# Optimization experiments

Hardware: AMD Instinct MI355X
Metric: run time of the kernel (lower is better)

Reference implementation:

```python
import jax, jax.numpy as jnp
import numpy as np

S, B, H = 2048, 2, 2048
NP = 16            # num attention heads
HN = H // NP       # head dim = 128


def setup_inputs() -> dict:
    key = jax.random.key(0)
    k0, k1, k2 = jax.random.split(key, 3)
    hidden_states = jax.random.normal(k0, (S, B, H), dtype=jnp.float32) * 0.02
    w_qkv = jax.random.normal(k1, (3 * H, H), dtype=jnp.float32) * 0.02
    b_qkv = jnp.zeros((3 * H,), dtype=jnp.float32)
    w_dense = jax.random.normal(k2, (H, H), dtype=jnp.float32) * 0.02
    b_dense = jnp.zeros((H,), dtype=jnp.float32)
    # causal mask: True means "mask out" (strictly upper triangular)
    attention_mask = jnp.triu(jnp.ones((S, S), dtype=bool), k=1)[None, None]  # [1,1,S,S]
    return {
        "hidden_states": hidden_states,
        "attention_mask": attention_mask,
        "w_qkv": w_qkv,
        "b_qkv": b_qkv,
        "w_dense": w_dense,
        "b_dense": b_dense,
    }


def reference(hidden_states, attention_mask, w_qkv, b_qkv, w_dense, b_dense):
    s, b, h = hidden_states.shape
    # fused QKV projection (ColumnParallelLinear: y = x @ W^T + b)
    mixed = hidden_states @ w_qkv.T + b_qkv                 # [s,b,3h]
    mixed = mixed.reshape(s, b, NP, 3 * HN)
    q, k, v = jnp.split(mixed, 3, axis=-1)                  # each [s,b,np,hn]
    norm = 1.0 / jnp.sqrt(jnp.asarray(HN, hidden_states.dtype))
    # scaled QK^T -> [b,np,sq,sk]
    scores = jnp.einsum("sbnh,tbnh->bnst", q, k) * norm
    # attention_mask_func: masked_fill(mask, -10000.0)
    scores = jnp.where(attention_mask, jnp.asarray(-10000.0, scores.dtype), scores)
    # softmax in fp32 (softmax_in_fp32)
    probs = jax.nn.softmax(scores.astype(jnp.float32), axis=-1).astype(scores.dtype)
    # AV matmul -> [s,b,np,hn] -> [s,b,h]
    context = jnp.einsum("bnst,tbnh->sbnh", probs, v).reshape(s, b, h)
    # output projection (RowParallelLinear)
    out = context @ w_dense.T + b_dense
    return out
```

## Files before the change

### kernel.cpp

```cpp
#include <hip/hip_runtime.h>
#include <hip/hip_bf16.h>
#include <cstdint>
#include <cstddef>

#define SS   2048
#define BB   2
#define HH   2048
#define NHEAD 16
#define HDIM 128
#define H3   6144
#define MROWS 4096

typedef __attribute__((ext_vector_type(4))) float f32x4;
typedef __attribute__((ext_vector_type(8))) __bf16 bf16x8;
typedef __attribute__((ext_vector_type(8))) unsigned short us8;
typedef __attribute__((ext_vector_type(4))) unsigned short us4;

__device__ __forceinline__ unsigned short f2b(float f) {
    union { float f; unsigned u; } v; v.f = f;
    unsigned r = v.u + 0x7fffu + ((v.u >> 16) & 1u);
    return (unsigned short)(r >> 16);
}

__device__ __forceinline__ bf16x8 ld_b16x8(const unsigned short* p) {
    us8 u = *(const us8*)p;
    return __builtin_bit_cast(bf16x8, u);
}

__device__ __forceinline__ bf16x8 ld8_off(const unsigned short* base, int byteoff) {
    return __builtin_bit_cast(bf16x8, *(const us8*)((const char*)base + byteoff));
}

__device__ __forceinline__ int sw256(int b) { return b ^ (((b >> 8) & 7) << 4); }
__device__ __forceinline__ int sw128(int b) { return b ^ (((b >> 7) & 7) << 4); }

__device__ __forceinline__ void gload_lds16(const unsigned short* g, unsigned short* l) {
    __builtin_amdgcn_global_load_lds(
        (const __attribute__((address_space(1))) unsigned int*)g,
        (__attribute__((address_space(3))) unsigned int*)l, 16, 0, 0);
}

__global__ __launch_bounds__(256) void cvt_f32_bf16(
    const float* __restrict__ in, unsigned short* __restrict__ out, int n4)
{
    const int stride = gridDim.x * blockDim.x;
    for (int i = blockIdx.x * blockDim.x + threadIdx.x; i < n4; i += stride) {
        const float4 v = ((const float4*)in)[i];
        us4 o = { f2b(v.x), f2b(v.y), f2b(v.z), f2b(v.w) };
        ((us4*)out)[i] = o;
    }
}

__global__ __launch_bounds__(256) void transpose_v(
    const unsigned short* __restrict__ mixed,
    unsigned short* __restrict__ vt)
{
    const int st = blockIdx.x;
    const int nh = blockIdx.y;
    const int bb = blockIdx.z;
    const int tid = threadIdx.x;
    __shared__ unsigned short T[64][136];
#pragma unroll
    for (int i = 0; i < 4; ++i) {
        const int c = i * 256 + tid;
        const int sl = c >> 4, d0 = (c & 15) << 3;
        const us8 v = *(const us8*)(mixed +
            ((size_t)(st * 64 + sl) * BB + bb) * H3 + nh * 384 + 256 + d0);
        *(us8*)(&T[sl][d0]) = v;
    }
    __syncthreads();
#pragma unroll
    for (int i = 0; i < 4; ++i) {
        const int c = i * 256 + tid;
        const int d = c >> 3, sl0 = (c & 7) << 3;
        us8 o;
#pragma unroll
        for (int j = 0; j < 8; ++j) o[j] = T[sl0 + j][d];
        *(us8*)(vt + ((size_t)(bb * NHEAD + nh) * HDIM + d) * SS + st * 64 + sl0) = o;
    }
}

#define STAGE_UNIT(gp, lo)                                        \
    gload_lds16((gp) + soff[0], smem + (lo) + tid * 8);           \
    gload_lds16((gp) + soff[1], smem + (lo) + 4096 + tid * 8);

template <int BN, bool F32OUT>
__global__ __launch_bounds__(512, 2) void gemm_8ph(
    const unsigned short* __restrict__ A,
    const unsigned short* __restrict__ Bw,
    const float* __restrict__ bias,
    void* __restrict__ Cout,
    int Nv, int Kv)
{
    extern __shared__ unsigned short smem[];
    constexpr int NF     = BN / 64;
    constexpr int BUNITS = BN / 128;
    constexpr int BELEMS = BN * 64;

    const int tid  = threadIdx.x;
    const int lane = tid & 63;
    const int wave = tid >> 6;
    const int wm = wave >> 2, wn = wave & 3;
    const int bm = blockIdx.y, bn = blockIdx.x;

    const unsigned short* Ab = A  + (size_t)bm * 128 * Kv;
    const unsigned short* Bb = Bw + (size_t)bn * BN * Kv;

    int soff[2];
#pragma unroll
    for (int i = 0; i < 2; ++i) {
        const int p = (i * 512 + tid) * 16;
        const int l = p ^ (((p >> 7) & 7) << 4);
        soff[i] = (l >> 7) * Kv + ((l & 127) >> 1);
    }

    f32x4 acc[4][NF];
#pragma unroll
    for (int m = 0; m < 4; ++m)
#pragma unroll
        for (int n = 0; n < NF; ++n) acc[m][n] = (f32x4){0.f, 0.f, 0.f, 0.f};

    const int frow = lane & 15;
    const int g16  = (lane >> 4) << 4;
    const int swx  = (frow & 7) << 4;
    const int kx0  = g16 ^ swx;
    const int kx1  = (64 + g16) ^ swx;
    const int aRow = (wm * 64 + frow) * 128;
    const int bRow = 32768 + (wn * (BN / 4) + frow) * 128;

    const int NT = Kv >> 6;

    STAGE_UNIT(Ab, 0);
    STAGE_UNIT(Bb, 16384);
    STAGE_UNIT(Bb + 128 * Kv, 16384 + 8192);
    if constexpr (BUNITS == 3) { STAGE_UNIT(Bb + 256 * Kv, 16384 + 16384); }
    STAGE_UNIT(Bb + 64, 16384 + BELEMS);
    STAGE_UNIT(Bb + 128 * Kv + 64, 16384 + BELEMS + 8192);
    if constexpr (BUNITS == 3) { STAGE_UNIT(Bb + 256 * Kv + 64, 16384 + BELEMS + 16384); }
    if constexpr (BUNITS == 3) { asm volatile("s_waitcnt vmcnt(6)" ::: "memory"); }
    else                       { asm volatile("s_waitcnt vmcnt(4)" ::: "memory"); }
    __builtin_amdgcn_s_barrier();

    for (int t = 0; t < NT; ++t) {
        const int j  = t & 1;
        const int jn = j ^ 1;
        const int aj = j * 16384;
        const int bj = j * (BN * 128);
        const int cA = ((t + 1 < NT) ? (t + 1) : (NT - 1)) * 64;
        const int cB = ((t + 2 < NT) ? (t + 2) : (NT - 1)) * 64;

        bf16x8 bbf[NF][2];

        {
            bf16x8 a0 = ld8_off(smem, aj + aRow + 0 * 2048 + kx0);
            bf16x8 a1 = ld8_off(smem, aj + aRow + 0 * 2048 + kx1);
#pragma unroll
            for (int n = 0; n < NF; ++n) {
                bbf[n][0] = ld8_off(smem, bj + bRow + n * 2048 + kx0);
                bbf[n][1] = ld8_off(smem, bj + bRow + n * 2048 + kx1);
            }
            STAGE_UNIT(Ab + cA, jn * 8192);
            __builtin_amdgcn_s_barrier();
            asm volatile("s_waitcnt lgkmcnt(0)" ::: "memory");
            __builtin_amdgcn_sched_barrier(0);
            __builtin_amdgcn_s_setprio(1);
#pragma unroll
            for (int n = 0; n < NF; ++n) {
                acc[0][n] = __builtin_amdgcn_mfma_f32_16x16x32_bf16(a0, bbf[n][0], acc[0][n], 0, 0, 0);
                acc[0][n] = __builtin_amdgcn_mfma_f32_16x16x32_bf16(a1, bbf[n][1], acc[0][n], 0, 0, 0);
            }
            __builtin_amdgcn_s_setprio(0);
        }
        {
            bf16x8 a0 = ld8_off(smem, aj + aRow + 1 * 2048 + kx0);
            bf16x8 a1 = ld8_off(smem, aj + aRow + 1 * 2048 + kx1);
            STAGE_UNIT(Bb + cB, 16384 + j * BELEMS);
            __builtin_amdgcn_s_barrier();
            asm volatile("s_waitcnt lgkmcnt(0)" ::: "memory");
            __builtin_amdgcn_sched_barrier(0);
            __builtin_amdgcn_s_setprio(1);
#pragma unroll
            for (int n = 0; n < NF; ++n) {
                acc[1][n] = __builtin_amdgcn_mfma_f32_16x16x32_bf16(a0, bbf[n][0], acc[1][n], 0, 0, 0);
                acc[1][n] = __builtin_amdgcn_mfma_f32_16x16x32_bf16(a1, bbf[n][1], acc[1][n], 0, 0, 0);
            }
            __builtin_amdgcn_s_setprio(0);
        }
        {
            bf16x8 a0 = ld8_off(smem, aj + aRow + 2 * 2048 + kx0);
            bf16x8 a1 = ld8_off(smem, aj + aRow + 2 * 2048 + kx1);
            STAGE_UNIT(Bb + 128 * Kv + cB, 16384 + j * BELEMS + 8192);
            __builtin_amdgcn_s_barrier();
            asm volatile("s_waitcnt lgkmcnt(0)" ::: "memory");
            __builtin_amdgcn_sched_barrier(0);
            __builtin_amdgcn_s_setprio(1);
#pragma unroll
            for (int n = 0; n < NF; ++n) {
                acc[2][n] = __builtin_amdgcn_mfma_f32_16x16x32_bf16(a0, bbf[n][0], acc[2][n], 0, 0, 0);
                acc[2][n] = __builtin_amdgcn_mfma_f32_16x16x32_bf16(a1, bbf[n][1], acc[2][n], 0, 0, 0);
            }
            __builtin_amdgcn_s_setprio(0);
        }
        {
            bf16x8 a0 = ld8_off(smem, aj + aRow + 3 * 2048 + kx0);
            bf16x8 a1 = ld8_off(smem, aj + aRow + 3 * 2048 + kx1);
            if constexpr (BUNITS == 3) {
                STAGE_UNIT(Bb + 256 * Kv + cB, 16384 + j * BELEMS + 16384);
            }
            __builtin_amdgcn_s_barrier();
            asm volatile("s_waitcnt lgkmcnt(0)" ::: "memory");
            __builtin_amdgcn_sched_barrier(0);
            __builtin_amdgcn_s_setprio(1);
#pragma unroll
            for (int n = 0; n < NF; ++n) {
                acc[3][n] = __builtin_amdgcn_mfma_f32_16x16x32_bf16(a0, bbf[n][0], acc[3][n], 0, 0, 0);
                acc[3][n] = __builtin_amdgcn_mfma_f32_16x16x32_bf16(a1, bbf[n][1], acc[3][n], 0, 0, 0);
            }
            __builtin_amdgcn_s_setprio(0);
            if constexpr (BUNITS == 3) { asm volatile("s_waitcnt vmcnt(6)" ::: "memory"); }
            else                       { asm volatile("s_waitcnt vmcnt(4)" ::: "memory"); }
        }
    }

    const int r0 = (lane >> 4) << 2;
#pragma unroll
    for (int m = 0; m < 4; ++m) {
        const int row = bm * 128 + wm * 64 + m * 16 + r0;
#pragma unroll
        for (int n = 0; n < NF; ++n) {
            const int col = bn * BN + wn * (BN / 4) + n * 16 + frow;
            const float bv = bias[col];
            float scale = 1.0f;
            if constexpr (!F32OUT) {
                if ((col % 384) < 128) scale = 0.088388347648318447f;
            }
#pragma unroll
            for (int r = 0; r < 4; ++r) {
                const float o = (acc[m][n][r] + bv) * scale;
                if (F32OUT) ((float*)Cout)[(size_t)(row + r) * Nv + col] = o;
                else        ((unsigned short*)Cout)[(size_t)(row + r) * Nv + col] = f2b(o);
            }
        }
    }
}

__global__ __launch_bounds__(256) void attn_kernel(
    const unsigned short* __restrict__ mixed,
    const unsigned short* __restrict__ vt,
    unsigned short* __restrict__ context)
{
    const int pair = blockIdx.x;
    const int nh   = blockIdx.y;
    const int bb   = blockIdx.z;
    const int tid  = threadIdx.x;
    const int lane = tid & 63;
    const int wave = tid >> 6;

    __shared__ __align__(1024) unsigned short smem[16384 + 16384 + 4096];

    const int frow = lane & 15;
    const int g16  = (lane >> 4) << 4;
    const int r0   = (lane >> 4) << 2;

    int koff[4], voff[4];
#pragma unroll
    for (int i = 0; i < 4; ++i) {
        const int p0 = (i * 256 + tid) * 16;
        const int lK = p0 ^ (((p0 >> 8) & 7) << 4);
        koff[i] = (lK >> 8) * (BB * H3) + ((lK & 255) >> 1);
        const int lV = p0 ^ (((p0 >> 7) & 7) << 4);
        voff[i] = (lV >> 7) * SS + ((lV & 127) >> 1);
    }

    const unsigned short* kg = mixed + (size_t)bb * H3 + nh * 384 + 128;
    const unsigned short* vg = vt + (size_t)(bb * NHEAD + nh) * HDIM * SS;

    char* Pb = (char*)(smem + 32768) + wave * 2048;

    for (int half = 0; half < 2; ++half) {
        const int qt = half ? (31 - pair) : pair;
        const int q0 = qt * 64 + wave * 16;

        bf16x8 qf[4];
        {
            const unsigned short* qptr =
                mixed + ((size_t)(q0 + frow) * BB + bb) * H3 + nh * 384;
#pragma unroll
            for (int kk = 0; kk < 4; ++kk)
                qf[kk] = ld_b16x8(qptr + kk * 32 + ((lane >> 4) << 3));
        }

        f32x4 Oacc[8];
#pragma unroll
        for (int ct = 0; ct < 8; ++ct) Oacc[ct] = (f32x4){0.f, 0.f, 0.f, 0.f};
        float m_r[4] = {-1e30f, -1e30f, -1e30f, -1e30f};
        float l_r[4] = {0.f, 0.f, 0.f, 0.f};

        {
            unsigned short* Kd = smem + wave * 512;
            unsigned short* Vd = smem + 16384 + wave * 512;
#pragma unroll
            for (int i = 0; i < 4; ++i) {
                gload_lds16(kg + koff[i], Kd + i * 2048);
                gload_lds16(vg + voff[i], Vd + i * 2048);
            }
        }
        __syncthreads();

        int cur = 0;
        for (int kt = 0; kt <= qt; ++kt) {
            if (kt < qt) {
                const unsigned short* kt_g = kg + (size_t)(kt + 1) * 64 * (BB * H3);
                const unsigned short* vt_g = vg + (kt + 1) * 64;
                unsigned short* Kd = smem + (cur ^ 1) * 8192 + wave * 512;
                unsigned short* Vd = smem + 16384 + (cur ^ 1) * 8192 + wave * 512;
#pragma unroll
                for (int i = 0; i < 4; ++i) {
                    gload_lds16(kt_g + koff[i], Kd + i * 2048);
                    gload_lds16(vt_g + voff[i], Vd + i * 2048);
                }
            }

            const unsigned short* Ks = smem + cur * 8192;
            const unsigned short* Vs = smem + 16384 + cur * 8192;

            f32x4 sc4[4];
#pragma unroll
            for (int t = 0; t < 4; ++t) {
                f32x4 s = (f32x4){0.f, 0.f, 0.f, 0.f};
#pragma unroll
                for (int kk = 0; kk < 4; ++kk) {
                    bf16x8 kf = ld8_off(Ks, sw256((t * 16 + frow) * 256 + kk * 64 + g16));
                    s = __builtin_amdgcn_mfma_f32_16x16x32_bf16(qf[kk], kf, s, 0, 0, 0);
                }
                sc4[t] = s;
            }

            if (kt == qt) {
#pragma unroll
                for (int t = 0; t < 4; ++t) {
                    const int kcol = qt * 64 + t * 16 + frow;
#pragma unroll
                    for (int r = 0; r < 4; ++r)
                        if (kcol > q0 + r0 + r) sc4[t][r] = -1e30f;
                }
            }

            float tmax[4];
#pragma unroll
            for (int r = 0; r < 4; ++r)
                tmax[r] = fmaxf(fmaxf(sc4[0][r], sc4[1][r]), fmaxf(sc4[2][r], sc4[3][r]));
#pragma unroll
            for (int r = 0; r < 4; ++r) {
                tmax[r] = fmaxf(tmax[r], __shfl_xor(tmax[r], 1, 64));
                tmax[r] = fmaxf(tmax[r], __shfl_xor(tmax[r], 2, 64));
                tmax[r] = fmaxf(tmax[r], __shfl_xor(tmax[r], 4, 64));
                tmax[r] = fmaxf(tmax[r], __shfl_xor(tmax[r], 8, 64));
            }

            bool need = false;
#pragma unroll
            for (int r = 0; r < 4; ++r) need = need || (tmax[r] > m_r[r] + 8.0f);
            if (__any(need)) {
                float a_r[4];
#pragma unroll
                for (int r = 0; r < 4; ++r) {
                    const float mnew = fmaxf(m_r[r], tmax[r]);
                    a_r[r] = __expf(m_r[r] - mnew);
                    m_r[r] = mnew;
                    l_r[r] *= a_r[r];
                }
#pragma unroll
                for (int ct = 0; ct < 8; ++ct)
#pragma unroll
                    for (int r = 0; r < 4; ++r) Oacc[ct][r] *= a_r[r];
            }

            float rsum[4] = {0.f, 0.f, 0.f, 0.f};
#pragma unroll
            for (int t = 0; t < 4; ++t)
#pragma unroll
                for (int r = 0; r < 4; ++r) {
                    const float p = __expf(sc4[t][r] - m_r[r]);
                    sc4[t][r] = p;
                    rsum[r] += p;
                }
#pragma unroll
            for (int r = 0; r < 4; ++r) {
                rsum[r] += __shfl_xor(rsum[r], 1, 64);
                rsum[r] += __shfl_xor(rsum[r], 2, 64);
                rsum[r] += __shfl_xor(rsum[r], 4, 64);
                rsum[r] += __shfl_xor(rsum[r], 8, 64);
                l_r[r] += rsum[r];
            }

#pragma unroll
            for (int t = 0; t < 4; ++t)
#pragma unroll
                for (int r = 0; r < 4; ++r)
                    *(unsigned short*)(Pb + sw128((r0 + r) * 128 + (t * 16 + frow) * 2)) =
                        f2b(sc4[t][r]);

#pragma unroll
            for (int ks = 0; ks < 2; ++ks) {
                bf16x8 pf = ld8_off((const unsigned short*)Pb, sw128(frow * 128 + ks * 64 + g16));
#pragma unroll
                for (int ct = 0; ct < 8; ++ct) {
                    bf16x8 vf = ld8_off(Vs, sw128((ct * 16 + frow) * 128 + ks * 64 + g16));
                    Oacc[ct] = __builtin_amdgcn_mfma_f32_16x16x32_bf16(pf, vf, Oacc[ct], 0, 0, 0);
                }
            }

            __syncthreads();
            cur ^= 1;
        }

#pragma unroll
        for (int ct = 0; ct < 8; ++ct) {
            const int d = ct * 16 + frow;
#pragma unroll
            for (int r = 0; r < 4; ++r) {
                const float o = Oacc[ct][r] / l_r[r];
                const size_t row = (size_t)(q0 + r0 + r) * BB + bb;
                context[row * HH + nh * 128 + d] = f2b(o);
            }
        }
    }
}

extern "C" void kernel_launch(void* const* d_in, const int* in_sizes, int n_in,
                              void* d_out, int out_size, void* d_ws, size_t ws_size,
                              hipStream_t stream) {
    const float* hidden  = (const float*)d_in[0];
    const float* w_qkv   = (const float*)d_in[2];
    const float* b_qkv   = (const float*)d_in[3];
    const float* w_dense = (const float*)d_in[4];
    const float* b_dense = (const float*)d_in[5];
    float* out = (float*)d_out;

    unsigned short* mixed = (unsigned short*)d_ws;
    unsigned short* hb    = mixed + (size_t)MROWS * H3;
    unsigned short* wq    = hb + (size_t)MROWS * HH;
    unsigned short* wd    = wq + (size_t)H3 * HH;
    unsigned short* context = hb;
    unsigned short* vtg     = wq;

    dim3 blk(256);
    cvt_f32_bf16<<<2048, blk, 0, stream>>>(hidden, hb, (MROWS * HH) / 4);
    cvt_f32_bf16<<<2048, blk, 0, stream>>>(w_qkv, wq, (H3 * HH) / 4);
    cvt_f32_bf16<<<1024, blk, 0, stream>>>(w_dense, wd, (HH * HH) / 4);

    hipFuncSetAttribute(reinterpret_cast<const void*>(gemm_8ph<384, false>),
                        hipFuncAttributeMaxDynamicSharedMemorySize, 131072);
    gemm_8ph<384, false><<<dim3(H3 / 384, MROWS / 128), dim3(512), 131072, stream>>>(
        hb, wq, b_qkv, mixed, H3, HH);
    transpose_v<<<dim3(32, NHEAD, BB), blk, 0, stream>>>(mixed, vtg);
    attn_kernel<<<dim3(16, NHEAD, BB), blk, 0, stream>>>(mixed, vtg, context);
    hipFuncSetAttribute(reinterpret_cast<const void*>(gemm_8ph<256, true>),
                        hipFuncAttributeMaxDynamicSharedMemorySize, 98304);
    gemm_8ph<256, true><<<dim3(HH / 256, MROWS / 128), dim3(512), 98304, stream>>>(
        context, wd, b_dense, out, HH, HH);
}
```

Measured before the change: 266.2 us.

## Use exp2 with folded log2e scale, lazy rescale reductions, hw bf16 cast, remapped grid

The log2(e) factor is folded into the Q scaling in the QKV GEMM epilogue, so the attention softmax can call raw v_exp_f32 (exp2) instead of __expf. The cross-lane max reduction now runs only when some lane's partial max passes the threshold, and that threshold is raised to 11.5 in log2 units. Software bf16 rounding is replaced with the hardware conversion. The attention grid is flattened to 1D and remapped so that neighbouring blocks land on different head/batch pairs, which is meant to spread work across XCDs. The looser rescale threshold allows larger unnormalised exponentials, which carries some precision risk.

```diff
diff --git a/kernel.cpp b/kernel.cpp
--- a/kernel.cpp
+++ b/kernel.cpp
@@ -20,6 +20,16 @@
     union { float f; unsigned u; } v; v.f = f;
     unsigned r = v.u + 0x7fffu + ((v.u >> 16) & 1u);
     return (unsigned short)(r >> 16);
+}
+
+__device__ __forceinline__ unsigned short f2b_hw(float f) {
+    return __builtin_bit_cast(unsigned short, (__bf16)f);
+}
+
+__device__ __forceinline__ float exp2_fast(float x) {
+    float r;
+    asm("v_exp_f32 %0, %1" : "=v"(r) : "v"(x));
+    return r;
 }
 
 __device__ __forceinline__ bf16x8 ld_b16x8(const unsigned short* p) {
@@ -232,7 +242,8 @@
             const float bv = bias[col];
             float scale = 1.0f;
             if constexpr (!F32OUT) {
-                if ((col % 384) < 128) scale = 0.088388347648318447f;
+                if ((col % 384) < 128)
+                    scale = (float)(0.08838834764831843 * 1.4426950408889634);
             }
 #pragma unroll
             for (int r = 0; r < 4; ++r) {
@@ -249,9 +260,14 @@
     const unsigned short* __restrict__ vt,
     unsigned short* __restrict__ context)
 {
-    const int pair = blockIdx.x;
-    const int nh   = blockIdx.y;
-    const int bb   = blockIdx.z;
+    const int id   = blockIdx.x;
+    const int c    = id & 7;
+    const int k    = id >> 3;
+    const int pair = k & 15;
+    const int nhbb = c + 8 * (k >> 4);
+    const int nh   = nhbb >> 1;
+    const int bb   = nhbb & 1;
+
     const int tid  = threadIdx.x;
     const int lane = tid & 63;
     const int wave = tid >> 6;
@@ -346,27 +362,28 @@
                 }
             }
 
-            float tmax[4];
+            float pmax[4];
 #pragma unroll
             for (int r = 0; r < 4; ++r)
-                tmax[r] = fmaxf(fmaxf(sc4[0][r], sc4[1][r]), fmaxf(sc4[2][r], sc4[3][r]));
-#pragma unroll
-            for (int r = 0; r < 4; ++r) {
-                tmax[r] = fmaxf(tmax[r], __shfl_xor(tmax[r], 1, 64));
-                tmax[r] = fmaxf(tmax[r], __shfl_xor(tmax[r], 2, 64));
-                tmax[r] = fmaxf(tmax[r], __shfl_xor(tmax[r], 4, 64));
-                tmax[r] = fmaxf(tmax[r], __shfl_xor(tmax[r], 8, 64));
-            }
-
+                pmax[r] = fmaxf(fmaxf(sc4[0][r], sc4[1][r]), fmaxf(sc4[2][r], sc4[3][r]));
             bool need = false;
 #pragma unroll
-            for (int r = 0; r < 4; ++r) need = need || (tmax[r] > m_r[r] + 8.0f);
+            for (int r = 0; r < 4; ++r) need = need || (pmax[r] > m_r[r] + 11.5f);
             if (__any(need)) {
+                float tmax[4];
+#pragma unroll
+                for (int r = 0; r < 4; ++r) {
+                    tmax[r] = pmax[r];
+                    tmax[r] = fmaxf(tmax[r], __shfl_xor(tmax[r], 1, 64));
+                    tmax[r] = fmaxf(tmax[r], __shfl_xor(tmax[r], 2, 64));
+                    tmax[r] = fmaxf(tmax[r], __shfl_xor(tmax[r], 4, 64));
+                    tmax[r] = fmaxf(tmax[r], __shfl_xor(tmax[r], 8, 64));
+                }
                 float a_r[4];
 #pragma unroll
                 for (int r = 0; r < 4; ++r) {
                     const float mnew = fmaxf(m_r[r], tmax[r]);
-                    a_r[r] = __expf(m_r[r] - mnew);
+                    a_r[r] = exp2_fast(m_r[r] - mnew);
                     m_r[r] = mnew;
                     l_r[r] *= a_r[r];
                 }
@@ -381,7 +398,7 @@
             for (int t = 0; t < 4; ++t)
 #pragma unroll
                 for (int r = 0; r < 4; ++r) {
-                    const float p = __expf(sc4[t][r] - m_r[r]);
+                    const float p = exp2_fast(sc4[t][r] - m_r[r]);
                     sc4[t][r] = p;
                     rsum[r] += p;
                 }
@@ -399,7 +416,7 @@
 #pragma unroll
                 for (int r = 0; r < 4; ++r)
                     *(unsigned short*)(Pb + sw128((r0 + r) * 128 + (t * 16 + frow) * 2)) =
-                        f2b(sc4[t][r]);
+                        f2b_hw(sc4[t][r]);
 
 #pragma unroll
             for (int ks = 0; ks < 2; ++ks) {
@@ -422,7 +439,7 @@
             for (int r = 0; r < 4; ++r) {
                 const float o = Oacc[ct][r] / l_r[r];
                 const size_t row = (size_t)(q0 + r0 + r) * BB + bb;
-                context[row * HH + nh * 128 + d] = f2b(o);
+                context[row * HH + nh * 128 + d] = f2b_hw(o);
             }
         }
     }
@@ -455,7 +472,7 @@
     gemm_8ph<384, false><<<dim3(H3 / 384, MROWS / 128), dim3(512), 131072, stream>>>(
         hb, wq, b_qkv, mixed, H3, HH);
     transpose_v<<<dim3(32, NHEAD, BB), blk, 0, stream>>>(mixed, vtg);
-    attn_kernel<<<dim3(16, NHEAD, BB), blk, 0, stream>>>(mixed, vtg, context);
+    attn_kernel<<<dim3(512), blk, 0, stream>>>(mixed, vtg, context);
     hipFuncSetAttribute(reinterpret_cast<const void*>(gemm_8ph<256, true>),
                         hipFuncAttributeMaxDynamicSharedMemorySize, 98304);
     gemm_8ph<256, true><<<dim3(HH / 256, MROWS / 128), dim3(512), 98304, stream>>>(
```

Measured after the change: 251.3 us. 5.6% less time.
